# Performance work log

Measured on AMD Instinct MI355X. Metric: run time of the kernel, lower is better.

Reference implementation:

```python
import jax, jax.numpy as jnp
import numpy as np

B, S, D, H, FF = 2, 2048, 1024, 16, 4096
DK = D // H
EPS = 1e-5


def setup_inputs() -> dict:
    key = jax.random.key(0)
    ks = jax.random.split(key, 16)
    sd = 0.02
    return {
        "x": jax.random.normal(ks[0], (B, S, D), jnp.float32),
        "mask": jnp.ones((B, 1, 1, S), jnp.int32),
        "wq_w": jax.random.normal(ks[1], (D, D), jnp.float32) * sd,
        "wq_b": jnp.zeros((D,), jnp.float32),
        "wk_w": jax.random.normal(ks[2], (D, D), jnp.float32) * sd,
        "wk_b": jnp.zeros((D,), jnp.float32),
        "wv_w": jax.random.normal(ks[3], (D, D), jnp.float32) * sd,
        "wv_b": jnp.zeros((D,), jnp.float32),
        "wo_w": jax.random.normal(ks[4], (D, D), jnp.float32) * sd,
        "wo_b": jnp.zeros((D,), jnp.float32),
        "ff1_w": jax.random.normal(ks[5], (FF, D), jnp.float32) * sd,
        "ff1_b": jnp.zeros((FF,), jnp.float32),
        "ff2_w": jax.random.normal(ks[6], (D, FF), jnp.float32) * sd,
        "ff2_b": jnp.zeros((D,), jnp.float32),
        "ln1_a": jnp.ones((D,), jnp.float32),
        "ln1_b": jnp.zeros((D,), jnp.float32),
        "ln2_a": jnp.ones((D,), jnp.float32),
        "ln2_b": jnp.zeros((D,), jnp.float32),
    }


def _layernorm(x, alpha, beta):
    # Matches torch module: std is unbiased (ddof=1), divides by (std + eps)
    mean = jnp.mean(x, -1, keepdims=True)
    std = jnp.std(x, -1, keepdims=True, ddof=1)
    return (x - mean) / (std + EPS) * alpha + beta


def _mha(x, mask, wq_w, wq_b, wk_w, wk_b, wv_w, wv_b, wo_w, wo_b):
    q = (x @ wq_w.T + wq_b).reshape(B, S, H, DK).transpose(0, 2, 1, 3)
    k = (x @ wk_w.T + wk_b).reshape(B, S, H, DK).transpose(0, 2, 1, 3)
    v = (x @ wv_w.T + wv_b).reshape(B, S, H, DK).transpose(0, 2, 1, 3)
    scores = jnp.einsum('bhqd,bhkd->bhqk', q, k) / jnp.sqrt(jnp.float32(DK))
    scores = jnp.where(mask == 0, -jnp.inf, scores)
    attn = jax.nn.softmax(scores, axis=-1)
    out = jnp.einsum('bhqk,bhkd->bhqd', attn, v)
    out = out.transpose(0, 2, 1, 3).reshape(B, S, D)
    return out @ wo_w.T + wo_b


def reference(x, mask, wq_w, wq_b, wk_w, wk_b, wv_w, wv_b, wo_w, wo_b,
              ff1_w, ff1_b, ff2_w, ff2_b, ln1_a, ln1_b, ln2_a, ln2_b):
    # Residual 1: pre-norm + self-attention (dropout = 0)
    h = _layernorm(x, ln1_a, ln1_b)
    x = x + _mha(h, mask, wq_w, wq_b, wk_w, wk_b, wv_w, wv_b, wo_w, wo_b)
    # Residual 2: pre-norm + FFN
    h = _layernorm(x, ln2_a, ln2_b)
    ff = jax.nn.relu(h @ ff1_w.T + ff1_b) @ ff2_w.T + ff2_b
    return x + ff
```

## Files before the change

kernel.cpp:

```cpp
#include <hip/hip_runtime.h>
#include <hip/hip_bf16.h>
#include <stdint.h>

#define B_   2
#define S_   2048
#define D_   1024
#define H_   16
#define FF_  4096
#define TOK  4096
#define EPS_ 1e-5f
#define SC2  0.18033688f

typedef __attribute__((ext_vector_type(8))) short short8;
typedef __attribute__((ext_vector_type(4))) short short4_t;
typedef __attribute__((ext_vector_type(4))) float float4_t;

__device__ __forceinline__ short f2bf(float f) {
  union { float f; uint32_t u; } v; v.f = f;
  uint32_t r = v.u + 0x7fffu + ((v.u >> 16) & 1u);
  return (short)(r >> 16);
}

__device__ __forceinline__ uint32_t pkbf(float a, float b) {
  __hip_bfloat162 h = __float22bfloat162_rn(make_float2(a, b));
  union { __hip_bfloat162 h; uint32_t u; } c; c.h = h; return c.u;
}

__device__ __forceinline__ void gload_lds16(const void* g, void* l) {
  __builtin_amdgcn_global_load_lds(
      (const __attribute__((address_space(1))) void*)g,
      (__attribute__((address_space(3))) void*)l, 16, 0, 0);
}

__global__ void cvt_all(const float* __restrict__ wq, const float* __restrict__ wk,
                        const float* __restrict__ wv, const float* __restrict__ wo,
                        const float* __restrict__ f1, const float* __restrict__ f2,
                        short* __restrict__ out) {
  const int n4 = (12 << 20) / 4;
  int idx = blockIdx.x * blockDim.x + threadIdx.x;
  int stride = gridDim.x * blockDim.x;
  for (int j4 = idx; j4 < n4; j4 += stride) {
    const int j = j4 * 4;
    const int seg = j >> 20;
    const float* src; int off;
    if (seg < 4)      { src = (seg == 0) ? wq : (seg == 1) ? wk : (seg == 2) ? wv : wo;
                        off = j & ((1 << 20) - 1); }
    else if (seg < 8) { src = f1; off = j - (4 << 20); }
    else              { src = f2; off = j - (8 << 20); }
    float4_t v = *(const float4_t*)(src + off);
    short4_t o = { f2bf(v[0]), f2bf(v[1]), f2bf(v[2]), f2bf(v[3]) };
    *(short4_t*)(out + j) = o;
  }
}

__global__ void mask_kernel(const int* __restrict__ m, float* __restrict__ o,
                            int* __restrict__ flags) {
  const int i = blockIdx.x * 64 + threadIdx.x;
  const int mv = m[i];
  o[i] = mv ? 0.0f : -1e30f;
  unsigned long long bal = __ballot(mv == 0);
  if (threadIdx.x == 0) flags[blockIdx.x] = (bal != 0ull) ? 1 : 0;
}

__global__ void combine_kernel(const float* __restrict__ x2, const float* __restrict__ p0,
                               float* __restrict__ out, const float* __restrict__ bias, int n) {
  int idx = blockIdx.x * blockDim.x + threadIdx.x;
  int stride = gridDim.x * blockDim.x;
  for (int j = idx * 4; j < n; j += stride * 4) {
    float4_t a = *(const float4_t*)(x2 + j);
    float4_t b = *(const float4_t*)(p0 + j);
    float4_t c = *(const float4_t*)(out + j);
    float4_t bb = *(const float4_t*)(bias + (j & (D_ - 1)));
    float4_t o = { a[0]+b[0]+c[0]+bb[0], a[1]+b[1]+c[1]+bb[1],
                   a[2]+b[2]+c[2]+bb[2], a[3]+b[3]+c[3]+bb[3] };
    *(float4_t*)(out + j) = o;
  }
}

__global__ __launch_bounds__(256) void ln_kernel(
    const float* __restrict__ x, const float* __restrict__ alpha,
    const float* __restrict__ beta, short* __restrict__ out)
{
  const int row = blockIdx.x;
  const int tid = threadIdx.x;
  const float4_t v = *(const float4_t*)(x + (size_t)row * D_ + tid * 4);
  float s  = v[0] + v[1] + v[2] + v[3];
  float ss = v[0]*v[0] + v[1]*v[1] + v[2]*v[2] + v[3]*v[3];
  #pragma unroll
  for (int m = 1; m < 64; m <<= 1) { s += __shfl_xor(s, m); ss += __shfl_xor(ss, m); }
  __shared__ float red[8];
  const int wave = tid >> 6, lane = tid & 63;
  if (lane == 0) { red[wave] = s; red[4 + wave] = ss; }
  __syncthreads();
  s  = red[0] + red[1] + red[2] + red[3];
  ss = red[4] + red[5] + red[6] + red[7];
  const float mean = s * (1.0f / D_);
  float var = (ss - (float)D_ * mean * mean) * (1.0f / (D_ - 1));
  var = fmaxf(var, 0.0f);
  const float inv = 1.0f / (sqrtf(var) + EPS_);
  short4_t o;
  #pragma unroll
  for (int j = 0; j < 4; j++) {
    float a = alpha[tid*4 + j], bb = beta[tid*4 + j];
    o[j] = f2bf((v[j] - mean) * inv * a + bb);
  }
  *(short4_t*)(out + (size_t)row * D_ + tid * 4) = o;
}

template<int EPI, int BN>
__global__ __launch_bounds__(256) void gemm_bt(
    const short* __restrict__ A, const short* __restrict__ Bm,
    void* __restrict__ Cout, void* __restrict__ Cout2,
    const float* __restrict__ bias, const float* __restrict__ res,
    int N, int K, int lda, int ldb)
{
  __shared__ __align__(16) short As[2][128][32];
  __shared__ __align__(16) short Bs[2][BN][32];

  const int tid  = threadIdx.x;
  const int wave = tid >> 6, lane = tid & 63;
  const int l15  = lane & 15, l4 = lane >> 4;

  const int gx = gridDim.x, gy = gridDim.y;
  int bid = (blockIdx.z * gy + blockIdx.y) * gx + blockIdx.x;
  const int q8 = (gx * gy * gridDim.z) >> 3;
  bid = (bid & 7) * q8 + (bid >> 3);
  const int n0 = (bid % gx) * BN;
  const int m0 = ((bid / gx) % gy) * 128;
  const int zi = bid / (gx * gy);
  const int koff = zi * K;

  constexpr int MI = (BN == 128) ? 4 : 2;
  const int rb = (BN == 128) ? (wave >> 1) * 64 : wave * 32;
  const int cb = (BN == 128) ? (wave & 1) * 64 : 0;

  float4_t acc[MI][4] = {};

  const int scol = (lane & 3) * 8;
  const short* gA0 = A + (size_t)(m0 + wave*32 + (lane >> 2)) * lda + koff + scol;
  const short* gA1 = gA0 + (size_t)16 * lda;
  const short* gB0;
  const short* gB1 = nullptr;
  if (BN == 128) {
    gB0 = Bm + (size_t)(n0 + wave*32 + (lane >> 2)) * ldb + koff + scol;
    gB1 = gB0 + (size_t)16 * ldb;
  } else {
    gB0 = Bm + (size_t)(n0 + wave*16 + (lane >> 2)) * ldb + koff + scol;
  }

  gload_lds16(gA0, &As[0][wave*32][0]);
  gload_lds16(gA1, &As[0][wave*32 + 16][0]);
  if (BN == 128) {
    gload_lds16(gB0, &Bs[0][wave*32][0]);
    gload_lds16(gB1, &Bs[0][wave*32 + 16][0]);
  } else {
    gload_lds16(gB0, &Bs[0][wave*16][0]);
  }

  for (int k0 = 0; k0 < K; k0 += 32) {
    const int cur = (k0 >> 5) & 1;
    __syncthreads();
    if (k0 + 32 < K) {
      gload_lds16(gA0 + k0 + 32, &As[cur^1][wave*32][0]);
      gload_lds16(gA1 + k0 + 32, &As[cur^1][wave*32 + 16][0]);
      if (BN == 128) {
        gload_lds16(gB0 + k0 + 32, &Bs[cur^1][wave*32][0]);
        gload_lds16(gB1 + k0 + 32, &Bs[cur^1][wave*32 + 16][0]);
      } else {
        gload_lds16(gB0 + k0 + 32, &Bs[cur^1][wave*16][0]);
      }
    }
    short8 af[MI], bf[4];
    #pragma unroll
    for (int i = 0; i < MI; i++)
      af[i] = *(const short8*)&As[cur][rb + i*16 + l15][l4*8];
    #pragma unroll
    for (int i = 0; i < 4; i++)
      bf[i] = *(const short8*)&Bs[cur][cb + i*16 + l15][l4*8];
    #pragma unroll
    for (int mi = 0; mi < MI; mi++)
      #pragma unroll
      for (int ni = 0; ni < 4; ni++)
        acc[mi][ni] = __builtin_amdgcn_mfma_f32_16x16x32_bf16(af[mi], bf[ni], acc[mi][ni], 0, 0, 0);
  }

  const int crow0 = m0 + rb + l4*4;
  const int ccol0 = n0 + cb + l15;
  float* dstf = (float*)((EPI == 4 && zi == 1) ? Cout2 : Cout);
  #pragma unroll
  for (int mi = 0; mi < MI; mi++) {
    #pragma unroll
    for (int ni = 0; ni < 4; ni++) {
      const int col = ccol0 + ni*16;
      const float bc = (EPI == 4) ? 0.0f : bias[col];
      #pragma unroll
      for (int r = 0; r < 4; r++) {
        const int row = crow0 + mi*16 + r;
        const float v = acc[mi][ni][r];
        if (EPI == 2) {
          ((short*)Cout)[(size_t)row * N + col] = f2bf(fmaxf(v + bc, 0.0f));
        } else if (EPI == 3) {
          ((float*)Cout)[(size_t)row * N + col] = res[(size_t)row * N + col] + v + bc;
        } else {
          dstf[(size_t)row * N + col] = v;
        }
      }
    }
  }
}

__global__ __launch_bounds__(256) void qkv_gemm(
    const short* __restrict__ A, const short* __restrict__ Bm,
    short* __restrict__ qkbuf, short* __restrict__ vt,
    const float* __restrict__ qb, const float* __restrict__ kb,
    const float* __restrict__ vb)
{
  __shared__ __align__(16) short As[2][128][32];
  __shared__ __align__(16) short Bs[2][128][32];

  const int tid  = threadIdx.x;
  const int wave = tid >> 6, lane = tid & 63;
  const int l15  = lane & 15, l4 = lane >> 4;

  const int gx = gridDim.x;
  int bid = blockIdx.y * gx + blockIdx.x;
  const int q8 = (gx * gridDim.y) >> 3;
  bid = (bid & 7) * q8 + (bid >> 3);
  const int n0 = (bid % gx) * 128;
  const int m0 = (bid / gx) * 128;

  const int rb = (wave >> 1) * 64;
  const int cb = (wave & 1) * 64;

  float4_t acc[4][4] = {};

  const int scol = (lane & 3) * 8;
  const short* gA0 = A  + (size_t)(m0 + wave*32 + (lane >> 2)) * 1024 + scol;
  const short* gA1 = gA0 + (size_t)16 * 1024;
  const short* gB0 = Bm + (size_t)(n0 + wave*32 + (lane >> 2)) * 1024 + scol;
  const short* gB1 = gB0 + (size_t)16 * 1024;

  gload_lds16(gA0, &As[0][wave*32][0]);
  gload_lds16(gA1, &As[0][wave*32 + 16][0]);
  gload_lds16(gB0, &Bs[0][wave*32][0]);
  gload_lds16(gB1, &Bs[0][wave*32 + 16][0]);

  for (int k0 = 0; k0 < 1024; k0 += 32) {
    const int cur = (k0 >> 5) & 1;
    __syncthreads();
    if (k0 + 32 < 1024) {
      gload_lds16(gA0 + k0 + 32, &As[cur^1][wave*32][0]);
      gload_lds16(gA1 + k0 + 32, &As[cur^1][wave*32 + 16][0]);
      gload_lds16(gB0 + k0 + 32, &Bs[cur^1][wave*32][0]);
      gload_lds16(gB1 + k0 + 32, &Bs[cur^1][wave*32 + 16][0]);
    }
    short8 af[4], bf[4];
    #pragma unroll
    for (int i = 0; i < 4; i++)
      af[i] = *(const short8*)&As[cur][rb + i*16 + l15][l4*8];
    #pragma unroll
    for (int i = 0; i < 4; i++)
      bf[i] = *(const short8*)&Bs[cur][cb + i*16 + l15][l4*8];
    #pragma unroll
    for (int mi = 0; mi < 4; mi++)
      #pragma unroll
      for (int ni = 0; ni < 4; ni++)
        acc[mi][ni] = __builtin_amdgcn_mfma_f32_16x16x32_bf16(af[mi], bf[ni], acc[mi][ni], 0, 0, 0);
  }

  const int crow0 = m0 + rb + l4*4;
  const int ccol0 = n0 + cb + l15;
  const int seg = n0 >> 10;
  if (seg < 2) {
    const float* bb = seg ? kb : qb;
    const float scl = seg ? 1.0f : SC2;
    #pragma unroll
    for (int mi = 0; mi < 4; mi++)
      #pragma unroll
      for (int ni = 0; ni < 4; ni++) {
        const int col = ccol0 + ni*16;
        const float bc = bb[col & 1023];
        #pragma unroll
        for (int r = 0; r < 4; r++)
          qkbuf[(size_t)(crow0 + mi*16 + r) * 2048 + col] =
              f2bf((acc[mi][ni][r] + bc) * scl);
      }
  } else {
    #pragma unroll
    for (int mi = 0; mi < 4; mi++)
      #pragma unroll
      for (int ni = 0; ni < 4; ni++) {
        const int d = ccol0 + ni*16 - 2048;
        const float bc = vb[d];
        short4_t o = { f2bf(acc[mi][ni][0] + bc), f2bf(acc[mi][ni][1] + bc),
                       f2bf(acc[mi][ni][2] + bc), f2bf(acc[mi][ni][3] + bc) };
        *(short4_t*)&vt[(size_t)d * TOK + crow0 + mi*16] = o;
      }
  }
}

__global__ __launch_bounds__(256, 4) void attn_kernel(
    const short* __restrict__ qk, const short* __restrict__ vt,
    const float* __restrict__ maskb, const int* __restrict__ mflags,
    short* __restrict__ out)
{
  int bid = (blockIdx.z * H_ + blockIdx.y) * (S_/64) + blockIdx.x;
  bid = (bid & 7) * ((B_ * H_ * (S_/64)) >> 3) + (bid >> 3);
  const int qt = bid % (S_/64);
  const int h  = (bid / (S_/64)) % H_;
  const int b  = bid / ((S_/64) * H_);

  const int tid = threadIdx.x, wave = tid >> 6, lane = tid & 63;
  const int l15 = lane & 15, l4 = lane >> 4;
  const int q0 = qt * 64 + wave * 16;

  __shared__ __align__(16) short Kt[2][4096];
  __shared__ __align__(16) short Vt[2][4096];

  short8 qa[2];
  #pragma unroll
  for (int kc = 0; kc < 2; kc++)
    qa[kc] = *(const short8*)&qk[(size_t)(b*S_ + q0 + l15) * 2048 + h*64 + kc*32 + l4*8];

  short8 ones;
  #pragma unroll
  for (int i = 0; i < 8; i++) ones[i] = (short)0x3F80;

  float4_t acc[4];
  #pragma unroll
  for (int dg = 0; dg < 4; dg++) acc[dg] = (float4_t){0.f, 0.f, 0.f, 0.f};
  float4_t accl = (float4_t){0.f, 0.f, 0.f, 0.f};
  float m2 = 0.0f;

  const int r8 = lane >> 3;
  const int ch = (lane & 7) ^ ((r8 & 3) | ((wave & 1) << 2));
  const int sbase = wave * 512;

  #pragma unroll
  for (int i = 0; i < 2; i++) {
    const int row = i*32 + wave*8 + r8;
    gload_lds16(qk + (size_t)(b*S_ + row) * 2048 + 1024 + h*64 + ch*8, &Kt[0][sbase + i*2048]);
    gload_lds16(vt + (size_t)(h*64 + row) * TOK + b*S_ + ch*8,         &Vt[0][sbase + i*2048]);
  }

  int krow[4];
  #pragma unroll
  for (int kg = 0; kg < 4; kg++)
    krow[kg] = 32*(kg>>1) + 8*(l15>>2) + 4*(kg&1) + (l15&3);
  const int gq = (l15 & 3) | (((l15 >> 2) & 1) << 2);
  const int gv = (l15 & 3) | (((l15 >> 3) & 1) << 2);

  for (int t = 0; t < S_/64; t++) {
    const int cur = t & 1;
    __syncthreads();
    if (t + 1 < S_/64) {
      const int k1 = (t + 1) * 64;
      #pragma unroll
      for (int i = 0; i < 2; i++) {
        const int row = i*32 + wave*8 + r8;
        gload_lds16(qk + (size_t)(b*S_ + k1 + row) * 2048 + 1024 + h*64 + ch*8, &Kt[cur^1][sbase + i*2048]);
        gload_lds16(vt + (size_t)(h*64 + row) * TOK + b*S_ + k1 + ch*8,         &Vt[cur^1][sbase + i*2048]);
      }
    }
    const short* Kc = &Kt[cur][0];
    const short* Vc = &Vt[cur][0];

    short8 kf[4][2], vf[4][2];
    #pragma unroll
    for (int kg = 0; kg < 4; kg++)
      #pragma unroll
      for (int kc = 0; kc < 2; kc++)
        kf[kg][kc] = *(const short8*)(Kc + krow[kg]*64 + ((l4 + kc*4) ^ gq) * 8);
    #pragma unroll
    for (int dg = 0; dg < 4; dg++)
      #pragma unroll
      for (int pc = 0; pc < 2; pc++)
        vf[dg][pc] = *(const short8*)(Vc + (dg*16 + l15)*64 + ((l4 + pc*4) ^ gv) * 8);

    const float negm2 = -m2;
    float4_t sc[4];
    #pragma unroll
    for (int kg = 0; kg < 4; kg++)
      sc[kg] = (float4_t){negm2, negm2, negm2, negm2};
    __builtin_amdgcn_s_setprio(1);
    #pragma unroll
    for (int kg = 0; kg < 4; kg++)
      #pragma unroll
      for (int kc = 0; kc < 2; kc++)
        sc[kg] = __builtin_amdgcn_mfma_f32_16x16x32_bf16(kf[kg][kc], qa[kc], sc[kg], 0, 0, 0);
    __builtin_amdgcn_s_setprio(0);

    if (mflags[b*(S_/64) + t]) {
      #pragma unroll
      for (int kg = 0; kg < 4; kg++) {
        float4_t mb = *(const float4_t*)&maskb[b*S_ + t*64 + 32*(kg>>1) + 4*(kg&1) + 8*l4];
        #pragma unroll
        for (int r = 0; r < 4; r++) sc[kg][r] += mb[r];
      }
    }

    float pm = fmaxf(fmaxf(sc[0][0], sc[0][1]), sc[0][2]);
    pm = fmaxf(fmaxf(pm, sc[0][3]), sc[1][0]);
    pm = fmaxf(fmaxf(pm, sc[1][1]), sc[1][2]);
    pm = fmaxf(fmaxf(pm, sc[1][3]), sc[2][0]);
    pm = fmaxf(fmaxf(pm, sc[2][1]), sc[2][2]);
    pm = fmaxf(fmaxf(pm, sc[2][3]), sc[3][0]);
    pm = fmaxf(fmaxf(pm, sc[3][1]), sc[3][2]);
    pm = fmaxf(pm, sc[3][3]);
    pm = fmaxf(pm, __shfl_xor(pm, 16));
    pm = fmaxf(pm, __shfl_xor(pm, 32));
    if (__any(pm > 8.0f)) {
      const float shift = fmaxf(pm, 0.0f);
      m2 += shift;
      const float esc = exp2f(-shift);
      #pragma unroll
      for (int r = 0; r < 4; r++) {
        const float er = __shfl(esc, l4*4 + r);
        #pragma unroll
        for (int dg = 0; dg < 4; dg++) acc[dg][r] *= er;
        accl[r] *= er;
      }
      #pragma unroll
      for (int kg = 0; kg < 4; kg++)
        #pragma unroll
        for (int r = 0; r < 4; r++) sc[kg][r] -= shift;
    }
    #pragma unroll
    for (int kg = 0; kg < 4; kg++)
      #pragma unroll
      for (int r = 0; r < 4; r++)
        sc[kg][r] = exp2f(sc[kg][r]);

    union { short8 s8; uint32_t u[4]; } pu[2];
    #pragma unroll
    for (int pc = 0; pc < 2; pc++) {
      pu[pc].u[0] = pkbf(sc[2*pc][0],   sc[2*pc][1]);
      pu[pc].u[1] = pkbf(sc[2*pc][2],   sc[2*pc][3]);
      pu[pc].u[2] = pkbf(sc[2*pc+1][0], sc[2*pc+1][1]);
      pu[pc].u[3] = pkbf(sc[2*pc+1][2], sc[2*pc+1][3]);
    }
    __builtin_amdgcn_s_setprio(1);
    #pragma unroll
    for (int dg = 0; dg < 4; dg++)
      #pragma unroll
      for (int pc = 0; pc < 2; pc++)
        acc[dg] = __builtin_amdgcn_mfma_f32_16x16x32_bf16(pu[pc].s8, vf[dg][pc], acc[dg], 0, 0, 0);
    #pragma unroll
    for (int pc = 0; pc < 2; pc++)
      accl = __builtin_amdgcn_mfma_f32_16x16x32_bf16(pu[pc].s8, ones, accl, 0, 0, 0);
    __builtin_amdgcn_s_setprio(0);
  }

  float linv[4];
  #pragma unroll
  for (int r = 0; r < 4; r++) linv[r] = 1.0f / accl[r];
  #pragma unroll
  for (int dg = 0; dg < 4; dg++)
    #pragma unroll
    for (int r = 0; r < 4; r++)
      out[(size_t)(b*S_ + q0 + l4*4 + r) * D_ + h*64 + dg*16 + l15] =
          f2bf(acc[dg][r] * linv[r]);
}

extern "C" void kernel_launch(void* const* d_in, const int* in_sizes, int n_in,
                              void* d_out, int out_size, void* d_ws, size_t ws_size,
                              hipStream_t stream)
{
  const float* x     = (const float*)d_in[0];
  const int*   mask  = (const int*)d_in[1];
  const float* wq_w  = (const float*)d_in[2];
  const float* wq_b  = (const float*)d_in[3];
  const float* wk_w  = (const float*)d_in[4];
  const float* wk_b  = (const float*)d_in[5];
  const float* wv_w  = (const float*)d_in[6];
  const float* wv_b  = (const float*)d_in[7];
  const float* wo_w  = (const float*)d_in[8];
  const float* wo_b  = (const float*)d_in[9];
  const float* ff1_w = (const float*)d_in[10];
  const float* ff1_b = (const float*)d_in[11];
  const float* ff2_w = (const float*)d_in[12];
  const float* ff2_b = (const float*)d_in[13];
  const float* ln1_a = (const float*)d_in[14];
  const float* ln1_b = (const float*)d_in[15];
  const float* ln2_a = (const float*)d_in[16];
  const float* ln2_b = (const float*)d_in[17];

  uint8_t* ws = (uint8_t*)d_ws;
  const size_t MB = 1024 * 1024;
  short* wqkv  = (short*)(ws + 0);
  short* wob   = (short*)(ws + 6*MB);
  short* ff1b  = (short*)(ws + 8*MB);
  short* ff2b  = (short*)(ws + 16*MB);
  float* maskb = (float*)(ws + 24*MB + 64*1024);
  int*   mflg  = (int*)(ws + 24*MB + 128*1024);
  short* h1    = (short*)(ws + 25*MB);
  short* qkbuf = (short*)(ws + 33*MB);
  short* vt    = (short*)(ws + 49*MB);
  short* attno = (short*)(ws + 57*MB);
  float* x2    = (float*)(ws + 65*MB);
  short* ffa   = (short*)(ws + 33*MB);
  float* p0    = (float*)(ws + 0);

  cvt_all<<<2048, 256, 0, stream>>>(wq_w, wk_w, wv_w, wo_w, ff1_w, ff2_w, (short*)ws);
  mask_kernel<<<TOK/64, 64, 0, stream>>>(mask, maskb, mflg);
  ln_kernel<<<TOK, 256, 0, stream>>>(x, ln1_a, ln1_b, h1);
  qkv_gemm<<<dim3(3072/128, TOK/128), 256, 0, stream>>>(
      h1, wqkv, qkbuf, vt, wq_b, wk_b, wv_b);
  attn_kernel<<<dim3(S_/64, H_, B_), 256, 0, stream>>>(qkbuf, vt, maskb, mflg, attno);
  gemm_bt<3,64><<<dim3(1024/64, TOK/128), 256, 0, stream>>>(
      attno, wob, x2, nullptr, wo_b, x, 1024, 1024, 1024, 1024);
  ln_kernel<<<TOK, 256, 0, stream>>>(x2, ln2_a, ln2_b, h1);
  gemm_bt<2,128><<<dim3(FF_/128, TOK/128), 256, 0, stream>>>(
      h1, ff1b, ffa, nullptr, ff1_b, nullptr, FF_, 1024, 1024, 1024);
  gemm_bt<4,128><<<dim3(1024/128, TOK/128, 2), 256, 0, stream>>>(
      ffa, ff2b, p0, d_out, nullptr, nullptr, 1024, 2048, FF_, FF_);
  combine_kernel<<<2048, 256, 0, stream>>>(x2, p0, (float*)d_out, ff2_b, TOK * D_);
}
```

Measured before the change: 284.9 us.

## Process two query sub-tiles per wave in attention, halving waves per block

The attention kernel now runs 2 waves per block, each handling 32 query rows (two 16-row MFMA tiles), instead of 4 waves with 16 rows each. Each K/V fragment read from LDS is reused across two query tiles, which cuts LDS read traffic per FLOP. The per-tile mask flags become a per-batch bitmask built with atomicOr after a memset, so the kernel reads one word per batch instead of one flag per tile. The trade is higher register pressure from doubled accumulators, fewer waves per block for latency hiding, and an extra memset launch.

```diff
diff --git a/kernel.cpp b/kernel.cpp
--- a/kernel.cpp
+++ b/kernel.cpp
@@ -54,12 +54,16 @@
 }
 
 __global__ void mask_kernel(const int* __restrict__ m, float* __restrict__ o,
-                            int* __restrict__ flags) {
+                            uint32_t* __restrict__ mbits) {
   const int i = blockIdx.x * 64 + threadIdx.x;
   const int mv = m[i];
   o[i] = mv ? 0.0f : -1e30f;
   unsigned long long bal = __ballot(mv == 0);
-  if (threadIdx.x == 0) flags[blockIdx.x] = (bal != 0ull) ? 1 : 0;
+  if (threadIdx.x == 0 && bal != 0ull) {
+    const int b = i >> 11;
+    const int t = (i >> 6) & 31;
+    atomicOr((unsigned int*)&mbits[b], 1u << t);
+  }
 }
 
 __global__ void combine_kernel(const float* __restrict__ x2, const float* __restrict__ p0,
@@ -299,9 +303,9 @@
   }
 }
 
-__global__ __launch_bounds__(256, 4) void attn_kernel(
+__global__ __launch_bounds__(128, 2) void attn_kernel(
     const short* __restrict__ qk, const short* __restrict__ vt,
-    const float* __restrict__ maskb, const int* __restrict__ mflags,
+    const float* __restrict__ maskb, const uint32_t* __restrict__ mbits,
     short* __restrict__ out)
 {
   int bid = (blockIdx.z * H_ + blockIdx.y) * (S_/64) + blockIdx.x;
@@ -312,35 +316,40 @@
 
   const int tid = threadIdx.x, wave = tid >> 6, lane = tid & 63;
   const int l15 = lane & 15, l4 = lane >> 4;
-  const int q0 = qt * 64 + wave * 16;
+  const int q0 = qt * 64 + wave * 32;
 
   __shared__ __align__(16) short Kt[2][4096];
   __shared__ __align__(16) short Vt[2][4096];
 
-  short8 qa[2];
-  #pragma unroll
-  for (int kc = 0; kc < 2; kc++)
-    qa[kc] = *(const short8*)&qk[(size_t)(b*S_ + q0 + l15) * 2048 + h*64 + kc*32 + l4*8];
+  short8 qa[2][2];
+  #pragma unroll
+  for (int mq = 0; mq < 2; mq++)
+    #pragma unroll
+    for (int kc = 0; kc < 2; kc++)
+      qa[mq][kc] = *(const short8*)&qk[(size_t)(b*S_ + q0 + mq*16 + l15) * 2048 + h*64 + kc*32 + l4*8];
 
   short8 ones;
   #pragma unroll
   for (int i = 0; i < 8; i++) ones[i] = (short)0x3F80;
 
-  float4_t acc[4];
-  #pragma unroll
-  for (int dg = 0; dg < 4; dg++) acc[dg] = (float4_t){0.f, 0.f, 0.f, 0.f};
-  float4_t accl = (float4_t){0.f, 0.f, 0.f, 0.f};
-  float m2 = 0.0f;
+  float4_t acc[2][4];
+  #pragma unroll
+  for (int mq = 0; mq < 2; mq++)
+    #pragma unroll
+    for (int dg = 0; dg < 4; dg++) acc[mq][dg] = (float4_t){0.f, 0.f, 0.f, 0.f};
+  float4_t accl[2] = {(float4_t){0.f,0.f,0.f,0.f}, (float4_t){0.f,0.f,0.f,0.f}};
+  float m2[2] = {0.0f, 0.0f};
+
+  const uint32_t mb32 = mbits[b];
 
   const int r8 = lane >> 3;
-  const int ch = (lane & 7) ^ ((r8 & 3) | ((wave & 1) << 2));
-  const int sbase = wave * 512;
-
-  #pragma unroll
-  for (int i = 0; i < 2; i++) {
-    const int row = i*32 + wave*8 + r8;
-    gload_lds16(qk + (size_t)(b*S_ + row) * 2048 + 1024 + h*64 + ch*8, &Kt[0][sbase + i*2048]);
-    gload_lds16(vt + (size_t)(h*64 + row) * TOK + b*S_ + ch*8,         &Vt[0][sbase + i*2048]);
+  const int ch = (lane & 7) ^ ((r8 & 3) | (wave << 2));
+
+  #pragma unroll
+  for (int i = 0; i < 4; i++) {
+    const int row = i*16 + wave*8 + r8;
+    gload_lds16(qk + (size_t)(b*S_ + row) * 2048 + 1024 + h*64 + ch*8, &Kt[0][(i*16 + wave*8)*64]);
+    gload_lds16(vt + (size_t)(h*64 + row) * TOK + b*S_ + ch*8,         &Vt[0][(i*16 + wave*8)*64]);
   }
 
   int krow[4];
@@ -356,110 +365,124 @@
     if (t + 1 < S_/64) {
       const int k1 = (t + 1) * 64;
       #pragma unroll
-      for (int i = 0; i < 2; i++) {
-        const int row = i*32 + wave*8 + r8;
-        gload_lds16(qk + (size_t)(b*S_ + k1 + row) * 2048 + 1024 + h*64 + ch*8, &Kt[cur^1][sbase + i*2048]);
-        gload_lds16(vt + (size_t)(h*64 + row) * TOK + b*S_ + k1 + ch*8,         &Vt[cur^1][sbase + i*2048]);
+      for (int i = 0; i < 4; i++) {
+        const int row = i*16 + wave*8 + r8;
+        gload_lds16(qk + (size_t)(b*S_ + k1 + row) * 2048 + 1024 + h*64 + ch*8, &Kt[cur^1][(i*16 + wave*8)*64]);
+        gload_lds16(vt + (size_t)(h*64 + row) * TOK + b*S_ + k1 + ch*8,         &Vt[cur^1][(i*16 + wave*8)*64]);
       }
     }
     const short* Kc = &Kt[cur][0];
     const short* Vc = &Vt[cur][0];
 
-    short8 kf[4][2], vf[4][2];
-    #pragma unroll
-    for (int kg = 0; kg < 4; kg++)
-      #pragma unroll
-      for (int kc = 0; kc < 2; kc++)
-        kf[kg][kc] = *(const short8*)(Kc + krow[kg]*64 + ((l4 + kc*4) ^ gq) * 8);
+    float4_t sc[2][4];
+    {
+      short8 kf[4][2];
+      #pragma unroll
+      for (int kg = 0; kg < 4; kg++)
+        #pragma unroll
+        for (int kc = 0; kc < 2; kc++)
+          kf[kg][kc] = *(const short8*)(Kc + krow[kg]*64 + ((l4 + kc*4) ^ gq) * 8);
+      #pragma unroll
+      for (int mq = 0; mq < 2; mq++) {
+        const float nm = -m2[mq];
+        #pragma unroll
+        for (int kg = 0; kg < 4; kg++) sc[mq][kg] = (float4_t){nm, nm, nm, nm};
+      }
+      __builtin_amdgcn_s_setprio(1);
+      #pragma unroll
+      for (int mq = 0; mq < 2; mq++)
+        #pragma unroll
+        for (int kg = 0; kg < 4; kg++)
+          #pragma unroll
+          for (int kc = 0; kc < 2; kc++)
+            sc[mq][kg] = __builtin_amdgcn_mfma_f32_16x16x32_bf16(kf[kg][kc], qa[mq][kc], sc[mq][kg], 0, 0, 0);
+      __builtin_amdgcn_s_setprio(0);
+    }
+
+    short8 vf[4][2];
     #pragma unroll
     for (int dg = 0; dg < 4; dg++)
       #pragma unroll
       for (int pc = 0; pc < 2; pc++)
         vf[dg][pc] = *(const short8*)(Vc + (dg*16 + l15)*64 + ((l4 + pc*4) ^ gv) * 8);
 
-    const float negm2 = -m2;
-    float4_t sc[4];
-    #pragma unroll
-    for (int kg = 0; kg < 4; kg++)
-      sc[kg] = (float4_t){negm2, negm2, negm2, negm2};
-    __builtin_amdgcn_s_setprio(1);
-    #pragma unroll
-    for (int kg = 0; kg < 4; kg++)
-      #pragma unroll
-      for (int kc = 0; kc < 2; kc++)
-        sc[kg] = __builtin_amdgcn_mfma_f32_16x16x32_bf16(kf[kg][kc], qa[kc], sc[kg], 0, 0, 0);
-    __builtin_amdgcn_s_setprio(0);
-
-    if (mflags[b*(S_/64) + t]) {
-      #pragma unroll
-      for (int kg = 0; kg < 4; kg++) {
-        float4_t mb = *(const float4_t*)&maskb[b*S_ + t*64 + 32*(kg>>1) + 4*(kg&1) + 8*l4];
-        #pragma unroll
-        for (int r = 0; r < 4; r++) sc[kg][r] += mb[r];
-      }
+    const bool mflag = (mb32 >> t) & 1u;
+
+    #pragma unroll
+    for (int mq = 0; mq < 2; mq++) {
+      if (mflag) {
+        #pragma unroll
+        for (int kg = 0; kg < 4; kg++) {
+          float4_t mb = *(const float4_t*)&maskb[b*S_ + t*64 + 32*(kg>>1) + 4*(kg&1) + 8*l4];
+          #pragma unroll
+          for (int r = 0; r < 4; r++) sc[mq][kg][r] += mb[r];
+        }
+      }
+      float pm = fmaxf(fmaxf(sc[mq][0][0], sc[mq][0][1]), sc[mq][0][2]);
+      pm = fmaxf(fmaxf(pm, sc[mq][0][3]), sc[mq][1][0]);
+      pm = fmaxf(fmaxf(pm, sc[mq][1][1]), sc[mq][1][2]);
+      pm = fmaxf(fmaxf(pm, sc[mq][1][3]), sc[mq][2][0]);
+      pm = fmaxf(fmaxf(pm, sc[mq][2][1]), sc[mq][2][2]);
+      pm = fmaxf(fmaxf(pm, sc[mq][2][3]), sc[mq][3][0]);
+      pm = fmaxf(fmaxf(pm, sc[mq][3][1]), sc[mq][3][2]);
+      pm = fmaxf(pm, sc[mq][3][3]);
+      pm = fmaxf(pm, __shfl_xor(pm, 16));
+      pm = fmaxf(pm, __shfl_xor(pm, 32));
+      if (__any(pm > 8.0f)) {
+        const float shift = fmaxf(pm, 0.0f);
+        m2[mq] += shift;
+        const float esc = exp2f(-shift);
+        #pragma unroll
+        for (int r = 0; r < 4; r++) {
+          const float er = __shfl(esc, l4*4 + r);
+          #pragma unroll
+          for (int dg = 0; dg < 4; dg++) acc[mq][dg][r] *= er;
+          accl[mq][r] *= er;
+        }
+        #pragma unroll
+        for (int kg = 0; kg < 4; kg++)
+          #pragma unroll
+          for (int r = 0; r < 4; r++) sc[mq][kg][r] -= shift;
+      }
+      #pragma unroll
+      for (int kg = 0; kg < 4; kg++)
+        #pragma unroll
+        for (int r = 0; r < 4; r++)
+          sc[mq][kg][r] = exp2f(sc[mq][kg][r]);
+
+      union { short8 s8; uint32_t u[4]; } pu[2];
+      #pragma unroll
+      for (int pc = 0; pc < 2; pc++) {
+        pu[pc].u[0] = pkbf(sc[mq][2*pc][0],   sc[mq][2*pc][1]);
+        pu[pc].u[1] = pkbf(sc[mq][2*pc][2],   sc[mq][2*pc][3]);
+        pu[pc].u[2] = pkbf(sc[mq][2*pc+1][0], sc[mq][2*pc+1][1]);
+        pu[pc].u[3] = pkbf(sc[mq][2*pc+1][2], sc[mq][2*pc+1][3]);
+      }
+      __builtin_amdgcn_s_setprio(1);
+      #pragma unroll
+      for (int dg = 0; dg < 4; dg++)
+        #pragma unroll
+        for (int pc = 0; pc < 2; pc++)
+          acc[mq][dg] = __builtin_amdgcn_mfma_f32_16x16x32_bf16(pu[pc].s8, vf[dg][pc], acc[mq][dg], 0, 0, 0);
+      #pragma unroll
+      for (int pc = 0; pc < 2; pc++)
+        accl[mq] = __builtin_amdgcn_mfma_f32_16x16x32_bf16(pu[pc].s8, ones, accl[mq], 0, 0, 0);
+      __builtin_amdgcn_s_setprio(0);
     }
-
-    float pm = fmaxf(fmaxf(sc[0][0], sc[0][1]), sc[0][2]);
-    pm = fmaxf(fmaxf(pm, sc[0][3]), sc[1][0]);
-    pm = fmaxf(fmaxf(pm, sc[1][1]), sc[1][2]);
-    pm = fmaxf(fmaxf(pm, sc[1][3]), sc[2][0]);
-    pm = fmaxf(fmaxf(pm, sc[2][1]), sc[2][2]);
-    pm = fmaxf(fmaxf(pm, sc[2][3]), sc[3][0]);
-    pm = fmaxf(fmaxf(pm, sc[3][1]), sc[3][2]);
-    pm = fmaxf(pm, sc[3][3]);
-    pm = fmaxf(pm, __shfl_xor(pm, 16));
-    pm = fmaxf(pm, __shfl_xor(pm, 32));
-    if (__any(pm > 8.0f)) {
-      const float shift = fmaxf(pm, 0.0f);
-      m2 += shift;
-      const float esc = exp2f(-shift);
-      #pragma unroll
-      for (int r = 0; r < 4; r++) {
-        const float er = __shfl(esc, l4*4 + r);
-        #pragma unroll
-        for (int dg = 0; dg < 4; dg++) acc[dg][r] *= er;
-        accl[r] *= er;
-      }
-      #pragma unroll
-      for (int kg = 0; kg < 4; kg++)
-        #pragma unroll
-        for (int r = 0; r < 4; r++) sc[kg][r] -= shift;
-    }
-    #pragma unroll
-    for (int kg = 0; kg < 4; kg++)
+  }
+
+  #pragma unroll
+  for (int mq = 0; mq < 2; mq++) {
+    float linv[4];
+    #pragma unroll
+    for (int r = 0; r < 4; r++) linv[r] = 1.0f / accl[mq][r];
+    #pragma unroll
+    for (int dg = 0; dg < 4; dg++)
       #pragma unroll
       for (int r = 0; r < 4; r++)
-        sc[kg][r] = exp2f(sc[kg][r]);
-
-    union { short8 s8; uint32_t u[4]; } pu[2];
-    #pragma unroll
-    for (int pc = 0; pc < 2; pc++) {
-      pu[pc].u[0] = pkbf(sc[2*pc][0],   sc[2*pc][1]);
-      pu[pc].u[1] = pkbf(sc[2*pc][2],   sc[2*pc][3]);
-      pu[pc].u[2] = pkbf(sc[2*pc+1][0], sc[2*pc+1][1]);
-      pu[pc].u[3] = pkbf(sc[2*pc+1][2], sc[2*pc+1][3]);
-    }
-    __builtin_amdgcn_s_setprio(1);
-    #pragma unroll
-    for (int dg = 0; dg < 4; dg++)
-      #pragma unroll
-      for (int pc = 0; pc < 2; pc++)
-        acc[dg] = __builtin_amdgcn_mfma_f32_16x16x32_bf16(pu[pc].s8, vf[dg][pc], acc[dg], 0, 0, 0);
-    #pragma unroll
-    for (int pc = 0; pc < 2; pc++)
-      accl = __builtin_amdgcn_mfma_f32_16x16x32_bf16(pu[pc].s8, ones, accl, 0, 0, 0);
-    __builtin_amdgcn_s_setprio(0);
-  }
-
-  float linv[4];
-  #pragma unroll
-  for (int r = 0; r < 4; r++) linv[r] = 1.0f / accl[r];
-  #pragma unroll
-  for (int dg = 0; dg < 4; dg++)
-    #pragma unroll
-    for (int r = 0; r < 4; r++)
-      out[(size_t)(b*S_ + q0 + l4*4 + r) * D_ + h*64 + dg*16 + l15] =
-          f2bf(acc[dg][r] * linv[r]);
+        out[(size_t)(b*S_ + q0 + mq*16 + l4*4 + r) * D_ + h*64 + dg*16 + l15] =
+            f2bf(acc[mq][dg][r] * linv[r]);
+  }
 }
 
 extern "C" void kernel_launch(void* const* d_in, const int* in_sizes, int n_in,
@@ -492,7 +515,7 @@
   short* ff1b  = (short*)(ws + 8*MB);
   short* ff2b  = (short*)(ws + 16*MB);
   float* maskb = (float*)(ws + 24*MB + 64*1024);
-  int*   mflg  = (int*)(ws + 24*MB + 128*1024);
+  uint32_t* mbits = (uint32_t*)(ws + 24*MB + 128*1024);
   short* h1    = (short*)(ws + 25*MB);
   short* qkbuf = (short*)(ws + 33*MB);
   short* vt    = (short*)(ws + 49*MB);
@@ -502,11 +525,12 @@
   float* p0    = (float*)(ws + 0);
 
   cvt_all<<<2048, 256, 0, stream>>>(wq_w, wk_w, wv_w, wo_w, ff1_w, ff2_w, (short*)ws);
-  mask_kernel<<<TOK/64, 64, 0, stream>>>(mask, maskb, mflg);
+  hipMemsetAsync(mbits, 0, B_ * sizeof(uint32_t), stream);
+  mask_kernel<<<TOK/64, 64, 0, stream>>>(mask, maskb, mbits);
   ln_kernel<<<TOK, 256, 0, stream>>>(x, ln1_a, ln1_b, h1);
   qkv_gemm<<<dim3(3072/128, TOK/128), 256, 0, stream>>>(
       h1, wqkv, qkbuf, vt, wq_b, wk_b, wv_b);
-  attn_kernel<<<dim3(S_/64, H_, B_), 256, 0, stream>>>(qkbuf, vt, maskb, mflg, attno);
+  attn_kernel<<<dim3(S_/64, H_, B_), 128, 0, stream>>>(qkbuf, vt, maskb, mbits, attno);
   gemm_bt<3,64><<<dim3(1024/64, TOK/128), 256, 0, stream>>>(
       attno, wob, x2, nullptr, wo_b, x, 1024, 1024, 1024, 1024);
   ln_kernel<<<TOK, 256, 0, stream>>>(x2, ln2_a, ln2_b, h1);
```

Result: slower. 313.2 us (+9.9%).

## Triple-buffer GEMM loads, split-K output projection, fuse residual with second layernorm

Applied to the files above, without the earlier changes.

The GEMM and QKV kernels move from a double-buffered LDS pipeline to a triple-buffered one, with explicit vmcnt waits and raw barriers so two tiles are in flight while one is computed. The output projection now uses 128-wide tiles with split-K over two partial buffers. A new ln2f kernel adds the residual, the bias and both partials, then applies the second layernorm in one pass, replacing the old residual epilogue plus a separate layernorm. The per-tile mask flags become a per-batch bitmask built with atomicOr after a memset. The extra LDS per block may lower occupancy, and the split-K path writes and reads extra fp32 partial buffers.

```diff
diff --git a/kernel.cpp b/kernel.cpp
--- a/kernel.cpp
+++ b/kernel.cpp
@@ -54,12 +54,16 @@
 }
 
 __global__ void mask_kernel(const int* __restrict__ m, float* __restrict__ o,
-                            int* __restrict__ flags) {
+                            uint32_t* __restrict__ mbits) {
   const int i = blockIdx.x * 64 + threadIdx.x;
   const int mv = m[i];
   o[i] = mv ? 0.0f : -1e30f;
   unsigned long long bal = __ballot(mv == 0);
-  if (threadIdx.x == 0) flags[blockIdx.x] = (bal != 0ull) ? 1 : 0;
+  if (threadIdx.x == 0 && bal != 0ull) {
+    const int b = i >> 11;
+    const int t = (i >> 6) & 31;
+    atomicOr((unsigned int*)&mbits[b], 1u << t);
+  }
 }
 
 __global__ void combine_kernel(const float* __restrict__ x2, const float* __restrict__ p0,
@@ -107,15 +111,53 @@
   *(short4_t*)(out + (size_t)row * D_ + tid * 4) = o;
 }
 
-template<int EPI, int BN>
+__global__ __launch_bounds__(256) void ln2f_kernel(
+    const float* __restrict__ p0, const float* __restrict__ p1,
+    const float* __restrict__ x, const float* __restrict__ ob,
+    const float* __restrict__ alpha, const float* __restrict__ beta,
+    float* __restrict__ x2, short* __restrict__ h2)
+{
+  const int row = blockIdx.x;
+  const int tid = threadIdx.x;
+  const size_t idx = (size_t)row * D_ + tid * 4;
+  float4_t a  = *(const float4_t*)(x  + idx);
+  float4_t b  = *(const float4_t*)(p0 + idx);
+  float4_t c  = *(const float4_t*)(p1 + idx);
+  float4_t bb = *(const float4_t*)(ob + tid * 4);
+  float4_t v = { a[0]+b[0]+c[0]+bb[0], a[1]+b[1]+c[1]+bb[1],
+                 a[2]+b[2]+c[2]+bb[2], a[3]+b[3]+c[3]+bb[3] };
+  *(float4_t*)(x2 + idx) = v;
+  float s  = v[0] + v[1] + v[2] + v[3];
+  float ss = v[0]*v[0] + v[1]*v[1] + v[2]*v[2] + v[3]*v[3];
+  #pragma unroll
+  for (int m = 1; m < 64; m <<= 1) { s += __shfl_xor(s, m); ss += __shfl_xor(ss, m); }
+  __shared__ float red[8];
+  const int wave = tid >> 6, lane = tid & 63;
+  if (lane == 0) { red[wave] = s; red[4 + wave] = ss; }
+  __syncthreads();
+  s  = red[0] + red[1] + red[2] + red[3];
+  ss = red[4] + red[5] + red[6] + red[7];
+  const float mean = s * (1.0f / D_);
+  float var = (ss - (float)D_ * mean * mean) * (1.0f / (D_ - 1));
+  var = fmaxf(var, 0.0f);
+  const float inv = 1.0f / (sqrtf(var) + EPS_);
+  short4_t o;
+  #pragma unroll
+  for (int j = 0; j < 4; j++) {
+    float al = alpha[tid*4 + j], be = beta[tid*4 + j];
+    o[j] = f2bf((v[j] - mean) * inv * al + be);
+  }
+  *(short4_t*)(h2 + idx) = o;
+}
+
+template<int EPI>
 __global__ __launch_bounds__(256) void gemm_bt(
     const short* __restrict__ A, const short* __restrict__ Bm,
     void* __restrict__ Cout, void* __restrict__ Cout2,
-    const float* __restrict__ bias, const float* __restrict__ res,
-    int N, int K, int lda, int ldb)
+    const float* __restrict__ bias, int N, int K, int lda, int ldb)
 {
-  __shared__ __align__(16) short As[2][128][32];
-  __shared__ __align__(16) short Bs[2][BN][32];
+  __shared__ __align__(16) short As[3][128][32];
+  __shared__ __align__(16) short Bs[3][128][32];
 
   const int tid  = threadIdx.x;
   const int wave = tid >> 6, lane = tid & 63;
@@ -125,70 +167,63 @@
   int bid = (blockIdx.z * gy + blockIdx.y) * gx + blockIdx.x;
   const int q8 = (gx * gy * gridDim.z) >> 3;
   bid = (bid & 7) * q8 + (bid >> 3);
-  const int n0 = (bid % gx) * BN;
+  const int n0 = (bid % gx) * 128;
   const int m0 = ((bid / gx) % gy) * 128;
   const int zi = bid / (gx * gy);
   const int koff = zi * K;
 
-  constexpr int MI = (BN == 128) ? 4 : 2;
-  const int rb = (BN == 128) ? (wave >> 1) * 64 : wave * 32;
-  const int cb = (BN == 128) ? (wave & 1) * 64 : 0;
-
-  float4_t acc[MI][4] = {};
+  const int rb = (wave >> 1) * 64;
+  const int cb = (wave & 1) * 64;
+
+  float4_t acc[4][4] = {};
 
   const int scol = (lane & 3) * 8;
   const short* gA0 = A + (size_t)(m0 + wave*32 + (lane >> 2)) * lda + koff + scol;
   const short* gA1 = gA0 + (size_t)16 * lda;
-  const short* gB0;
-  const short* gB1 = nullptr;
-  if (BN == 128) {
-    gB0 = Bm + (size_t)(n0 + wave*32 + (lane >> 2)) * ldb + koff + scol;
-    gB1 = gB0 + (size_t)16 * ldb;
-  } else {
-    gB0 = Bm + (size_t)(n0 + wave*16 + (lane >> 2)) * ldb + koff + scol;
-  }
-
-  gload_lds16(gA0, &As[0][wave*32][0]);
-  gload_lds16(gA1, &As[0][wave*32 + 16][0]);
-  if (BN == 128) {
-    gload_lds16(gB0, &Bs[0][wave*32][0]);
-    gload_lds16(gB1, &Bs[0][wave*32 + 16][0]);
-  } else {
-    gload_lds16(gB0, &Bs[0][wave*16][0]);
-  }
-
-  for (int k0 = 0; k0 < K; k0 += 32) {
-    const int cur = (k0 >> 5) & 1;
-    __syncthreads();
-    if (k0 + 32 < K) {
-      gload_lds16(gA0 + k0 + 32, &As[cur^1][wave*32][0]);
-      gload_lds16(gA1 + k0 + 32, &As[cur^1][wave*32 + 16][0]);
-      if (BN == 128) {
-        gload_lds16(gB0 + k0 + 32, &Bs[cur^1][wave*32][0]);
-        gload_lds16(gB1 + k0 + 32, &Bs[cur^1][wave*32 + 16][0]);
-      } else {
-        gload_lds16(gB0 + k0 + 32, &Bs[cur^1][wave*16][0]);
-      }
-    }
-    short8 af[MI], bf[4];
-    #pragma unroll
-    for (int i = 0; i < MI; i++)
+  const short* gB0 = Bm + (size_t)(n0 + wave*32 + (lane >> 2)) * ldb + koff + scol;
+  const short* gB1 = gB0 + (size_t)16 * ldb;
+
+#define STAGE_G(bf_, ko_) do { \
+    gload_lds16(gA0 + (ko_), &As[bf_][wave*32][0]); \
+    gload_lds16(gA1 + (ko_), &As[bf_][wave*32 + 16][0]); \
+    gload_lds16(gB0 + (ko_), &Bs[bf_][wave*32][0]); \
+    gload_lds16(gB1 + (ko_), &Bs[bf_][wave*32 + 16][0]); \
+  } while (0)
+
+  const int nt = K >> 5;
+  STAGE_G(0, 0);
+  STAGE_G(1, 32);
+
+  for (int t = 0; t < nt; ++t) {
+    if (t + 1 < nt) { asm volatile("s_waitcnt vmcnt(4)" ::: "memory"); }
+    else            { asm volatile("s_waitcnt vmcnt(0)" ::: "memory"); }
+    __builtin_amdgcn_s_barrier();
+    __builtin_amdgcn_sched_barrier(0);
+    if (t + 2 < nt) {
+      const int nb = (t + 2) % 3;
+      STAGE_G(nb, (t + 2) * 32);
+    }
+    const int cur = t % 3;
+    short8 af[4], bf[4];
+    #pragma unroll
+    for (int i = 0; i < 4; i++)
       af[i] = *(const short8*)&As[cur][rb + i*16 + l15][l4*8];
     #pragma unroll
     for (int i = 0; i < 4; i++)
       bf[i] = *(const short8*)&Bs[cur][cb + i*16 + l15][l4*8];
     #pragma unroll
-    for (int mi = 0; mi < MI; mi++)
+    for (int mi = 0; mi < 4; mi++)
       #pragma unroll
       for (int ni = 0; ni < 4; ni++)
         acc[mi][ni] = __builtin_amdgcn_mfma_f32_16x16x32_bf16(af[mi], bf[ni], acc[mi][ni], 0, 0, 0);
   }
+#undef STAGE_G
 
   const int crow0 = m0 + rb + l4*4;
   const int ccol0 = n0 + cb + l15;
   float* dstf = (float*)((EPI == 4 && zi == 1) ? Cout2 : Cout);
   #pragma unroll
-  for (int mi = 0; mi < MI; mi++) {
+  for (int mi = 0; mi < 4; mi++) {
     #pragma unroll
     for (int ni = 0; ni < 4; ni++) {
       const int col = ccol0 + ni*16;
@@ -199,8 +234,6 @@
         const float v = acc[mi][ni][r];
         if (EPI == 2) {
           ((short*)Cout)[(size_t)row * N + col] = f2bf(fmaxf(v + bc, 0.0f));
-        } else if (EPI == 3) {
-          ((float*)Cout)[(size_t)row * N + col] = res[(size_t)row * N + col] + v + bc;
         } else {
           dstf[(size_t)row * N + col] = v;
         }
@@ -215,8 +248,8 @@
     const float* __restrict__ qb, const float* __restrict__ kb,
     const float* __restrict__ vb)
 {
-  __shared__ __align__(16) short As[2][128][32];
-  __shared__ __align__(16) short Bs[2][128][32];
+  __shared__ __align__(16) short As[3][128][32];
+  __shared__ __align__(16) short Bs[3][128][32];
 
   const int tid  = threadIdx.x;
   const int wave = tid >> 6, lane = tid & 63;
@@ -240,20 +273,26 @@
   const short* gB0 = Bm + (size_t)(n0 + wave*32 + (lane >> 2)) * 1024 + scol;
   const short* gB1 = gB0 + (size_t)16 * 1024;
 
-  gload_lds16(gA0, &As[0][wave*32][0]);
-  gload_lds16(gA1, &As[0][wave*32 + 16][0]);
-  gload_lds16(gB0, &Bs[0][wave*32][0]);
-  gload_lds16(gB1, &Bs[0][wave*32 + 16][0]);
-
-  for (int k0 = 0; k0 < 1024; k0 += 32) {
-    const int cur = (k0 >> 5) & 1;
-    __syncthreads();
-    if (k0 + 32 < 1024) {
-      gload_lds16(gA0 + k0 + 32, &As[cur^1][wave*32][0]);
-      gload_lds16(gA1 + k0 + 32, &As[cur^1][wave*32 + 16][0]);
-      gload_lds16(gB0 + k0 + 32, &Bs[cur^1][wave*32][0]);
-      gload_lds16(gB1 + k0 + 32, &Bs[cur^1][wave*32 + 16][0]);
-    }
+#define STAGE_Q(bf_, ko_) do { \
+    gload_lds16(gA0 + (ko_), &As[bf_][wave*32][0]); \
+    gload_lds16(gA1 + (ko_), &As[bf_][wave*32 + 16][0]); \
+    gload_lds16(gB0 + (ko_), &Bs[bf_][wave*32][0]); \
+    gload_lds16(gB1 + (ko_), &Bs[bf_][wave*32 + 16][0]); \
+  } while (0)
+
+  STAGE_Q(0, 0);
+  STAGE_Q(1, 32);
+
+  for (int t = 0; t < 32; ++t) {
+    if (t + 1 < 32) { asm volatile("s_waitcnt vmcnt(4)" ::: "memory"); }
+    else            { asm volatile("s_waitcnt vmcnt(0)" ::: "memory"); }
+    __builtin_amdgcn_s_barrier();
+    __builtin_amdgcn_sched_barrier(0);
+    if (t + 2 < 32) {
+      const int nb = (t + 2) % 3;
+      STAGE_Q(nb, (t + 2) * 32);
+    }
+    const int cur = t % 3;
     short8 af[4], bf[4];
     #pragma unroll
     for (int i = 0; i < 4; i++)
@@ -267,6 +306,7 @@
       for (int ni = 0; ni < 4; ni++)
         acc[mi][ni] = __builtin_amdgcn_mfma_f32_16x16x32_bf16(af[mi], bf[ni], acc[mi][ni], 0, 0, 0);
   }
+#undef STAGE_Q
 
   const int crow0 = m0 + rb + l4*4;
   const int ccol0 = n0 + cb + l15;
@@ -301,7 +341,7 @@
 
 __global__ __launch_bounds__(256, 4) void attn_kernel(
     const short* __restrict__ qk, const short* __restrict__ vt,
-    const float* __restrict__ maskb, const int* __restrict__ mflags,
+    const float* __restrict__ maskb, const uint32_t* __restrict__ mbits,
     short* __restrict__ out)
 {
   int bid = (blockIdx.z * H_ + blockIdx.y) * (S_/64) + blockIdx.x;
@@ -332,6 +372,8 @@
   float4_t accl = (float4_t){0.f, 0.f, 0.f, 0.f};
   float m2 = 0.0f;
 
+  const uint32_t mb32 = mbits[b];
+
   const int r8 = lane >> 3;
   const int ch = (lane & 7) ^ ((r8 & 3) | ((wave & 1) << 2));
   const int sbase = wave * 512;
@@ -390,7 +432,7 @@
         sc[kg] = __builtin_amdgcn_mfma_f32_16x16x32_bf16(kf[kg][kc], qa[kc], sc[kg], 0, 0, 0);
     __builtin_amdgcn_s_setprio(0);
 
-    if (mflags[b*(S_/64) + t]) {
+    if ((mb32 >> t) & 1u) {
       #pragma unroll
       for (int kg = 0; kg < 4; kg++) {
         float4_t mb = *(const float4_t*)&maskb[b*S_ + t*64 + 32*(kg>>1) + 4*(kg&1) + 8*l4];
@@ -492,27 +534,30 @@
   short* ff1b  = (short*)(ws + 8*MB);
   short* ff2b  = (short*)(ws + 16*MB);
   float* maskb = (float*)(ws + 24*MB + 64*1024);
-  int*   mflg  = (int*)(ws + 24*MB + 128*1024);
+  uint32_t* mbits = (uint32_t*)(ws + 24*MB + 128*1024);
   short* h1    = (short*)(ws + 25*MB);
   short* qkbuf = (short*)(ws + 33*MB);
   short* vt    = (short*)(ws + 49*MB);
   short* attno = (short*)(ws + 57*MB);
   float* x2    = (float*)(ws + 65*MB);
+  float* p0w   = (float*)(ws + 33*MB);
+  float* p1w   = (float*)(ws + 49*MB);
   short* ffa   = (short*)(ws + 33*MB);
-  float* p0    = (float*)(ws + 0);
+  float* p0f   = (float*)(ws + 0);
 
   cvt_all<<<2048, 256, 0, stream>>>(wq_w, wk_w, wv_w, wo_w, ff1_w, ff2_w, (short*)ws);
-  mask_kernel<<<TOK/64, 64, 0, stream>>>(mask, maskb, mflg);
+  hipMemsetAsync(mbits, 0, B_ * sizeof(uint32_t), stream);
+  mask_kernel<<<TOK/64, 64, 0, stream>>>(mask, maskb, mbits);
   ln_kernel<<<TOK, 256, 0, stream>>>(x, ln1_a, ln1_b, h1);
   qkv_gemm<<<dim3(3072/128, TOK/128), 256, 0, stream>>>(
       h1, wqkv, qkbuf, vt, wq_b, wk_b, wv_b);
-  attn_kernel<<<dim3(S_/64, H_, B_), 256, 0, stream>>>(qkbuf, vt, maskb, mflg, attno);
-  gemm_bt<3,64><<<dim3(1024/64, TOK/128), 256, 0, stream>>>(
-      attno, wob, x2, nullptr, wo_b, x, 1024, 1024, 1024, 1024);
-  ln_kernel<<<TOK, 256, 0, stream>>>(x2, ln2_a, ln2_b, h1);
-  gemm_bt<2,128><<<dim3(FF_/128, TOK/128), 256, 0, stream>>>(
-      h1, ff1b, ffa, nullptr, ff1_b, nullptr, FF_, 1024, 1024, 1024);
-  gemm_bt<4,128><<<dim3(1024/128, TOK/128, 2), 256, 0, stream>>>(
-      ffa, ff2b, p0, d_out, nullptr, nullptr, 1024, 2048, FF_, FF_);
-  combine_kernel<<<2048, 256, 0, stream>>>(x2, p0, (float*)d_out, ff2_b, TOK * D_);
-}
+  attn_kernel<<<dim3(S_/64, H_, B_), 256, 0, stream>>>(qkbuf, vt, maskb, mbits, attno);
+  gemm_bt<4><<<dim3(1024/128, TOK/128, 2), 256, 0, stream>>>(
+      attno, wob, p0w, p1w, nullptr, 1024, 512, 1024, 1024);
+  ln2f_kernel<<<TOK, 256, 0, stream>>>(p0w, p1w, x, wo_b, ln2_a, ln2_b, x2, h1);
+  gemm_bt<2><<<dim3(FF_/128, TOK/128), 256, 0, stream>>>(
+      h1, ff1b, ffa, nullptr, ff1_b, FF_, 1024, 1024, 1024);
+  gemm_bt<4><<<dim3(1024/128, TOK/128, 2), 256, 0, stream>>>(
+      ffa, ff2b, p0f, d_out, nullptr, 1024, 2048, FF_, FF_);
+  combine_kernel<<<2048, 256, 0, stream>>>(x2, p0f, (float*)d_out, ff2_b, TOK * D_);
+}
```

Result: slower. 294.6 us (+3.4%).
